# Kernel tuning notes

Hardware: AMD Instinct MI355X
Metric: run time of the kernel (lower is better)

The kernel has to match this reference:

```python
import jax, jax.numpy as jnp
import numpy as np

BS, L, D, N, K = 2048, 100, 256, 16, 32
M_CONST = 2
NEG = -1e9


def setup_inputs() -> dict:
    key = jax.random.key(0)
    ks = jax.random.split(key, 6)
    hist = jax.random.normal(ks[0], (BS, L, D), dtype=jnp.float32)
    hist_mask = jnp.ones((BS, L), dtype=jnp.float32)  # passed but unused by PolyAttention (faithful)
    cand = jax.random.normal(ks[1], (BS, N, D), dtype=jnp.float32)
    num_interests = jax.random.randint(ks[2], (BS,), 1, K + 1, dtype=jnp.int32)
    cat_counts = jax.random.randint(ks[3], (BS,), 1, 21, dtype=jnp.int32)
    W_poly = jax.random.normal(ks[4], (D, D), dtype=jnp.float32) * (1.0 / np.sqrt(D))
    context_codes = jax.random.normal(ks[5], (K, D), dtype=jnp.float32) * (1.0 / np.sqrt(D))
    return {
        "history_news_representations": hist,
        "history_mask": hist_mask,
        "candidate_news_representations": cand,
        "num_extracted_interests": num_interests,
        "unique_category_counts": cat_counts,
        "W_poly": W_poly,
        "context_codes": context_codes,
    }


def _forward(hist, hist_mask, cand, num_interests, cat_counts, W_poly, context_codes):
    # --- PolyAttention ---
    proj = jnp.tanh(jnp.einsum("bld,ed->ble", hist, W_poly))        # [bs, L, ccd]
    weights = jnp.einsum("ble,ke->bkl", proj, context_codes)         # [bs, K, L]
    cc_mask = jnp.arange(K)[None, :] < num_interests[:, None]        # [bs, K]
    weights = jnp.where(cc_mask[:, :, None], weights, NEG)
    weights = jax.nn.softmax(weights, axis=2)
    weights = jnp.nan_to_num(weights, nan=0.0, posinf=0.0, neginf=0.0)
    interests = jnp.einsum("bkl,bld->bkd", weights, hist)            # [bs, K, d]

    # --- InterestCandidateAttention over all N candidates at once ---
    aw = jnp.einsum("bkd,bnd->bnk", interests, cand)                 # [bs, N, K]
    dyn_K = jnp.ceil(jnp.log2(M_CONST * cat_counts.astype(jnp.float32))).astype(jnp.int32)
    dyn_K = jnp.clip(dyn_K, 1, K)                                    # [bs]
    # rank of each entry in descending order along K
    order = jnp.argsort(-aw, axis=-1)
    rank = jnp.argsort(order, axis=-1)                               # [bs, N, K]
    topk_mask = (rank < dyn_K[:, None, None]).astype(aw.dtype)
    masked = aw * topk_mask
    user = jnp.einsum("bnk,bkd->bnd", masked, interests)             # [bs, N, d]
    return user


def reference(history_news_representations, history_mask, candidate_news_representations,
              num_extracted_interests, unique_category_counts, W_poly, context_codes):
    return _forward(history_news_representations, history_mask, candidate_news_representations,
                    num_extracted_interests, unique_category_counts, W_poly, context_codes)
```

## Files before the change

kernel.cpp:

```cpp
#include <hip/hip_runtime.h>
#include <math.h>

#define NEGV (-1e9f)

typedef _Float16 half8 __attribute__((ext_vector_type(8)));
typedef float f32x4 __attribute__((ext_vector_type(4)));


__device__ inline float tanh_fast(float x) {
    float t = __expf(2.0f * x);
    float r = __builtin_amdgcn_rcpf(t + 1.0f);
    return fmaf(-2.0f, r, 1.0f);
}

__device__ inline void split8(const float4 a, const float4 b, half8& h, half8& m) {
    const float* pa = (const float*)&a;
    const float* pb = (const float*)&b;
    #pragma unroll
    for (int q = 0; q < 4; ++q) {
        float x = pa[q];
        _Float16 hi = (_Float16)x;
        h[q] = hi; m[q] = (_Float16)(x - (float)hi);
    }
    #pragma unroll
    for (int q = 0; q < 4; ++q) {
        float x = pb[q];
        _Float16 hi = (_Float16)x;
        h[4+q] = hi; m[4+q] = (_Float16)(x - (float)hi);
    }
}

__device__ inline void gload_lds16(const void* g, void* lds) {
    __builtin_amdgcn_global_load_lds(
        (const __attribute__((address_space(1))) unsigned int*)g,
        (__attribute__((address_space(3))) unsigned int*)lds, 16, 0, 0);
}

__global__ __launch_bounds__(256)
void k_prep(const float* __restrict__ W, const float* __restrict__ cc,
            half8* __restrict__ Wf, half8* __restrict__ Cf)
{
    int slot = blockIdx.x * 256 + threadIdx.x;
    if (slot < 8192) {
        int kt = slot >> 10;
        int ct = (slot >> 6) & 15;
        int lane = slot & 63;
        int e = ct * 16 + (lane & 15);
        int g = lane >> 4;
        const float* src = &W[(size_t)e * 256 + kt * 32 + g * 8];
        float4 a = *(const float4*)src;
        float4 b = *(const float4*)(src + 4);
        half8 h, m;
        split8(a, b, h, m);
        Wf[((kt * 2 + 0) * 16 + ct) * 64 + lane] = h;
        Wf[((kt * 2 + 1) * 16 + ct) * 64 + lane] = m;
    } else if (slot < 9216) {
        int s = slot - 8192;
        int lane = s & 63;
        int ct = (s >> 6) & 1;
        int et = s >> 7;
        int k2 = ct * 16 + (lane & 15);
        int g = lane >> 4;
        const float* src = &cc[(size_t)k2 * 256 + et * 32 + g * 8];
        float4 a = *(const float4*)src;
        float4 b = *(const float4*)(src + 4);
        half8 h, m;
        split8(a, b, h, m);
        Cf[((et * 2 + 0) * 2 + ct) * 64 + lane] = h;
        Cf[((et * 2 + 1) * 2 + ct) * 64 + lane] = m;
    }
}

__global__ __launch_bounds__(512, 2)
void k_proj_logits(const float* __restrict__ hist, const half8* __restrict__ Wf,
                   const half8* __restrict__ Cf, float* __restrict__ logits)
{
    __shared__ __align__(16) char smem[65536];
    float (*Pj)[68] = (float(*)[68])smem;

    const int tid  = threadIdx.x;
    const int lane = tid & 63;
    const int w    = tid >> 6;
    const int wr   = w >> 1, wc = w & 1;
    const int g    = lane >> 4;
    const int r    = lane & 15;
    const size_t rowBase = (size_t)blockIdx.x * 256;

    f32x4 acc[4][8];
    #pragma unroll
    for (int i = 0; i < 4; ++i)
        #pragma unroll
        for (int j = 0; j < 8; ++j) acc[i][j] = (f32x4)(0.0f);

    const float* aPtr = &hist[(rowBase + (size_t)wr * 64 + r) * 256 + g * 8];
    const char*  wsrc = (const char*)Wf + tid * 16;
    const int    ldsW = (tid & 448) * 16;

    float4 a0[4], a1[4];
    #pragma unroll
    for (int rt = 0; rt < 4; ++rt) {
        const float* s = aPtr + rt * (16 * 256);
        a0[rt] = *(const float4*)s;
        a1[rt] = *(const float4*)(s + 4);
    }
    #pragma unroll
    for (int i = 0; i < 4; ++i)
        gload_lds16(wsrc + i * 8192, smem + ldsW + i * 8192);
    __syncthreads();

    #pragma unroll 2
    for (int kt = 0; kt < 8; ++kt) {
        const int cur = kt & 1;
        if (kt < 7) {
            const char* s = wsrc + (size_t)(kt + 1) * 32768;
            char* d = smem + (cur ^ 1) * 32768 + ldsW;
            #pragma unroll
            for (int i = 0; i < 4; ++i)
                gload_lds16(s + i * 8192, d + i * 8192);
        }
        half8 Ah[4], Am[4];
        #pragma unroll
        for (int rt = 0; rt < 4; ++rt)
            split8(a0[rt], a1[rt], Ah[rt], Am[rt]);
        if (kt < 7) {
            #pragma unroll
            for (int rt = 0; rt < 4; ++rt) {
                const float* s = aPtr + rt * (16 * 256) + (kt + 1) * 32;
                a0[rt] = *(const float4*)s;
                a1[rt] = *(const float4*)(s + 4);
            }
        }
        __builtin_amdgcn_sched_barrier(0);

        const _Float16* Bf = (const _Float16*)(smem + cur * 32768);
        #pragma unroll
        for (int ct = 0; ct < 8; ++ct) {
            int ctg = wc * 8 + ct;
            half8 Bh = *(const half8*)&Bf[(( 0 + ctg) * 64 + lane) * 8];
            half8 Bm = *(const half8*)&Bf[((16 + ctg) * 64 + lane) * 8];
            #pragma unroll
            for (int rt = 0; rt < 4; ++rt) {
                acc[rt][ct] = __builtin_amdgcn_mfma_f32_16x16x32_f16(Ah[rt], Bh, acc[rt][ct], 0, 0, 0);
                acc[rt][ct] = __builtin_amdgcn_mfma_f32_16x16x32_f16(Ah[rt], Bm, acc[rt][ct], 0, 0, 0);
                acc[rt][ct] = __builtin_amdgcn_mfma_f32_16x16x32_f16(Am[rt], Bh, acc[rt][ct], 0, 0, 0);
            }
        }
        __syncthreads();
    }

    #pragma unroll
    for (int p = 0; p < 2; ++p) {
        f32x4 acc2[2];
        acc2[0] = (f32x4)(0.0f);
        acc2[1] = (f32x4)(0.0f);
        #pragma unroll
        for (int ec = 0; ec < 4; ++ec) {
            __syncthreads();
            if ((wr >> 1) == p && wc == (ec >> 1)) {
                #pragma unroll
                for (int rt = 0; rt < 4; ++rt) {
                    #pragma unroll
                    for (int c4i = 0; c4i < 4; ++c4i) {
                        int ctm = (ec & 1) * 4 + c4i;
                        f32x4 t = acc[rt][ctm];
                        int el = c4i * 16 + r;
                        int rb = (wr & 1) * 64 + rt * 16 + g * 4;
                        #pragma unroll
                        for (int i = 0; i < 4; ++i)
                            Pj[rb + i][el] = tanh_fast(t[i]);
                    }
                }
            }
            __syncthreads();
            #pragma unroll
            for (int ks = 0; ks < 2; ++ks) {
                half8 Ah2, Am2;
                {
                    const float* src = &Pj[w * 16 + r][ks * 32 + g * 8];
                    float4 p0 = *(const float4*)src;
                    float4 p1 = *(const float4*)(src + 4);
                    split8(p0, p1, Ah2, Am2);
                }
                int et = ec * 2 + ks;
                #pragma unroll
                for (int ct = 0; ct < 2; ++ct) {
                    half8 Bh = Cf[((et * 2 + 0) * 2 + ct) * 64 + lane];
                    half8 Bm = Cf[((et * 2 + 1) * 2 + ct) * 64 + lane];
                    acc2[ct] = __builtin_amdgcn_mfma_f32_16x16x32_f16(Ah2, Bh, acc2[ct], 0, 0, 0);
                    acc2[ct] = __builtin_amdgcn_mfma_f32_16x16x32_f16(Ah2, Bm, acc2[ct], 0, 0, 0);
                    acc2[ct] = __builtin_amdgcn_mfma_f32_16x16x32_f16(Am2, Bh, acc2[ct], 0, 0, 0);
                }
            }
        }
        #pragma unroll
        for (int ct = 0; ct < 2; ++ct)
            #pragma unroll
            for (int i = 0; i < 4; ++i) {
                size_t grow = rowBase + p * 128 + w * 16 + g * 4 + i;
                logits[grow * 32 + ct * 16 + r] = acc2[ct][i];
            }
    }
}

__global__ __launch_bounds__(256, 3)
void k_attn(const float* __restrict__ hist, const float* __restrict__ cand,
            const int* __restrict__ numi, const int* __restrict__ catc,
            const float* __restrict__ logits, float* __restrict__ out)
{
    __shared__ float wT[100][36];
    __shared__ float ints[32][260];
    __shared__ float aws[16][36];
    __shared__ float maw[16][36];

    const int tid = threadIdx.x;
    const int b = blockIdx.x;
    const int num = numi[b];

    for (int idx = tid; idx < 3200; idx += 256) {
        int l = idx >> 5;
        int k = idx & 31;
        wT[l][k] = logits[(size_t)b * 3200 + idx];
    }
    __syncthreads();

    {
        const int k = tid >> 3;
        const int lg = tid & 7;
        const bool valid = k < num;
        float vals[13];
        float m = -INFINITY;
        #pragma unroll
        for (int i = 0; i < 13; ++i) {
            int l = lg + 8 * i;
            if (l < 100) {
                float v = valid ? wT[l][k] : NEGV;
                vals[i] = v;
                m = fmaxf(m, v);
            }
        }
        #pragma unroll
        for (int off = 1; off < 8; off <<= 1)
            m = fmaxf(m, __shfl_xor(m, off, 8));
        float s = 0.0f;
        #pragma unroll
        for (int i = 0; i < 13; ++i) {
            int l = lg + 8 * i;
            if (l < 100) {
                float e = expf(vals[i] - m);
                s += e;
                wT[l][k] = e;
            }
        }
        #pragma unroll
        for (int off = 1; off < 8; off <<= 1)
            s += __shfl_xor(s, off, 8);
        float inv = 1.0f / s;
        #pragma unroll
        for (int i = 0; i < 13; ++i) {
            int l = lg + 8 * i;
            if (l < 100) wT[l][k] *= inv;
        }
    }
    __syncthreads();

    {
        const int dq = tid & 63;
        const int kh = tid >> 6;
        float4 a4[8];
        #pragma unroll
        for (int kk = 0; kk < 8; ++kk) { a4[kk].x = a4[kk].y = a4[kk].z = a4[kk].w = 0.0f; }
        const float4* hrow = (const float4*)&hist[(size_t)b * 25600] + dq;
        #pragma unroll 4
        for (int l = 0; l < 100; ++l) {
            float4 hv = hrow[(size_t)l * 64];
            float4 w0 = *(const float4*)&wT[l][8 * kh];
            float4 w1 = *(const float4*)&wT[l][8 * kh + 4];
            float wv[8] = {w0.x, w0.y, w0.z, w0.w, w1.x, w1.y, w1.z, w1.w};
            #pragma unroll
            for (int kk = 0; kk < 8; ++kk) {
                a4[kk].x = fmaf(wv[kk], hv.x, a4[kk].x);
                a4[kk].y = fmaf(wv[kk], hv.y, a4[kk].y);
                a4[kk].z = fmaf(wv[kk], hv.z, a4[kk].z);
                a4[kk].w = fmaf(wv[kk], hv.w, a4[kk].w);
            }
        }
        #pragma unroll
        for (int kk = 0; kk < 8; ++kk)
            *(float4*)&ints[8 * kh + kk][4 * dq] = a4[kk];
    }
    __syncthreads();

    {
        const int n = tid & 15;
        const int kq = tid >> 4;
        const float4* cg = (const float4*)&cand[((size_t)b * 16 + n) * 256];
        const float4* i0 = (const float4*)&ints[kq][0];
        const float4* i1 = (const float4*)&ints[kq + 16][0];
        float s0 = 0.0f, s1 = 0.0f;
        for (int q = 0; q < 64; ++q) {
            float4 cv = cg[q];
            float4 v0 = i0[q];
            float4 v1 = i1[q];
            s0 += v0.x * cv.x + v0.y * cv.y + v0.z * cv.z + v0.w * cv.w;
            s1 += v1.x * cv.x + v1.y * cv.y + v1.z * cv.z + v1.w * cv.w;
        }
        aws[n][kq] = s0;
        aws[n][kq + 16] = s1;
    }
    __syncthreads();

    {
        int c = catc[b];
        int dynK = 32 - __clz(2 * c - 1);
        const int k = tid & 31;
        const int n1 = tid >> 5;
        #pragma unroll
        for (int h = 0; h < 2; ++h) {
            int n = n1 + 8 * h;
            float a = aws[n][k];
            int cnt = 0;
            #pragma unroll
            for (int j = 0; j < 32; ++j) {
                float aj = aws[n][j];
                cnt += (aj > a) || (aj == a && j < k);
            }
            maw[n][k] = (cnt < dynK) ? a : 0.0f;
        }
    }
    __syncthreads();

    {
        const int dd = tid & 63;
        const int ng = tid >> 6;
        float4 acc4[4];
        #pragma unroll
        for (int nn = 0; nn < 4; ++nn) { acc4[nn].x = acc4[nn].y = acc4[nn].z = acc4[nn].w = 0.0f; }
        for (int k = 0; k < 32; ++k) {
            float4 iv = *(const float4*)&ints[k][4 * dd];
            #pragma unroll
            for (int nn = 0; nn < 4; ++nn) {
                float m = maw[4 * ng + nn][k];
                acc4[nn].x = fmaf(m, iv.x, acc4[nn].x);
                acc4[nn].y = fmaf(m, iv.y, acc4[nn].y);
                acc4[nn].z = fmaf(m, iv.z, acc4[nn].z);
                acc4[nn].w = fmaf(m, iv.w, acc4[nn].w);
            }
        }
        #pragma unroll
        for (int nn = 0; nn < 4; ++nn) {
            *(float4*)&out[((size_t)b * 16 + 4 * ng + nn) * 256 + 4 * dd] = acc4[nn];
        }
    }
}

extern "C" void kernel_launch(void* const* d_in, const int* in_sizes, int n_in,
                              void* d_out, int out_size, void* d_ws, size_t ws_size,
                              hipStream_t stream) {
    const float* hist = (const float*)d_in[0];
    const float* cand = (const float*)d_in[2];
    const int*   numi = (const int*)d_in[3];
    const int*   catc = (const int*)d_in[4];
    const float* W    = (const float*)d_in[5];
    const float* cc   = (const float*)d_in[6];
    float* out = (float*)d_out;
    float* logits = (float*)d_ws;
    const size_t LOG_BYTES = 26214400;
    const size_t WF_BYTES = 262144;
    const size_t CF_BYTES = 32768;
    char* fragBase = (ws_size >= LOG_BYTES + WF_BYTES + CF_BYTES)
                     ? ((char*)d_ws + LOG_BYTES)
                     : (char*)d_out;
    half8* Wf = (half8*)fragBase;
    half8* Cf = (half8*)(fragBase + WF_BYTES);

    k_prep<<<36, 256, 0, stream>>>(W, cc, Wf, Cf);
    k_proj_logits<<<800, 512, 0, stream>>>(hist, Wf, Cf, logits);
    k_attn<<<2048, 256, 0, stream>>>(hist, cand, numi, catc, logits, out);
}
```

Baseline: 276.7 us.

## Interleave projection GEMM with fine-grained barriers, packed fp16 split, and aliased attention LDS

The projection GEMM main loop is split into four sub-phases per k-tile. Each sub-phase loads B fragments ahead, raises wave priority around the MFMA bursts, and uses explicit vmcnt waits and raw s_barriers instead of full __syncthreads. The fp32-to-fp16 hi/lo split now uses packed cvt_pkrtz conversions, which switch rounding to round-toward-zero and may shift accuracy slightly. The attention kernel aliases the wT and ints shared buffers, adding one barrier, so its LDS footprint drops enough to allow 4 blocks per CU instead of 3.

```diff
diff --git a/kernel.cpp b/kernel.cpp
--- a/kernel.cpp
+++ b/kernel.cpp
@@ -4,6 +4,7 @@
 #define NEGV (-1e9f)
 
 typedef _Float16 half8 __attribute__((ext_vector_type(8)));
+typedef __fp16 fp16x2 __attribute__((ext_vector_type(2)));
 typedef float f32x4 __attribute__((ext_vector_type(4)));
 
 
@@ -14,19 +15,15 @@
 }
 
 __device__ inline void split8(const float4 a, const float4 b, half8& h, half8& m) {
-    const float* pa = (const float*)&a;
-    const float* pb = (const float*)&b;
+    const float x[8] = {a.x, a.y, a.z, a.w, b.x, b.y, b.z, b.w};
     #pragma unroll
     for (int q = 0; q < 4; ++q) {
-        float x = pa[q];
-        _Float16 hi = (_Float16)x;
-        h[q] = hi; m[q] = (_Float16)(x - (float)hi);
-    }
-    #pragma unroll
-    for (int q = 0; q < 4; ++q) {
-        float x = pb[q];
-        _Float16 hi = (_Float16)x;
-        h[4+q] = hi; m[4+q] = (_Float16)(x - (float)hi);
+        fp16x2 hp = __builtin_amdgcn_cvt_pkrtz(x[2 * q], x[2 * q + 1]);
+        float r0 = x[2 * q]     - (float)hp[0];
+        float r1 = x[2 * q + 1] - (float)hp[1];
+        fp16x2 mp = __builtin_amdgcn_cvt_pkrtz(r0, r1);
+        h[2 * q] = (_Float16)hp[0]; h[2 * q + 1] = (_Float16)hp[1];
+        m[2 * q] = (_Float16)mp[0]; m[2 * q + 1] = (_Float16)mp[1];
     }
 }
 
@@ -106,46 +103,65 @@
     #pragma unroll
     for (int i = 0; i < 4; ++i)
         gload_lds16(wsrc + i * 8192, smem + ldsW + i * 8192);
-    __syncthreads();
-
-    #pragma unroll 2
+    __builtin_amdgcn_sched_barrier(0);
+    asm volatile("s_waitcnt vmcnt(0)" ::: "memory");
+    __builtin_amdgcn_s_barrier();
+    __builtin_amdgcn_sched_barrier(0);
+
     for (int kt = 0; kt < 8; ++kt) {
         const int cur = kt & 1;
-        if (kt < 7) {
-            const char* s = wsrc + (size_t)(kt + 1) * 32768;
-            char* d = smem + (cur ^ 1) * 32768 + ldsW;
-            #pragma unroll
-            for (int i = 0; i < 4; ++i)
-                gload_lds16(s + i * 8192, d + i * 8192);
-        }
+        const _Float16* Bf = (const _Float16*)(smem + cur * 32768);
         half8 Ah[4], Am[4];
         #pragma unroll
-        for (int rt = 0; rt < 4; ++rt)
-            split8(a0[rt], a1[rt], Ah[rt], Am[rt]);
-        if (kt < 7) {
-            #pragma unroll
-            for (int rt = 0; rt < 4; ++rt) {
-                const float* s = aPtr + rt * (16 * 256) + (kt + 1) * 32;
-                a0[rt] = *(const float4*)s;
-                a1[rt] = *(const float4*)(s + 4);
-            }
-        }
-        __builtin_amdgcn_sched_barrier(0);
-
-        const _Float16* Bf = (const _Float16*)(smem + cur * 32768);
-        #pragma unroll
-        for (int ct = 0; ct < 8; ++ct) {
-            int ctg = wc * 8 + ct;
-            half8 Bh = *(const half8*)&Bf[(( 0 + ctg) * 64 + lane) * 8];
-            half8 Bm = *(const half8*)&Bf[((16 + ctg) * 64 + lane) * 8];
-            #pragma unroll
-            for (int rt = 0; rt < 4; ++rt) {
-                acc[rt][ct] = __builtin_amdgcn_mfma_f32_16x16x32_f16(Ah[rt], Bh, acc[rt][ct], 0, 0, 0);
-                acc[rt][ct] = __builtin_amdgcn_mfma_f32_16x16x32_f16(Ah[rt], Bm, acc[rt][ct], 0, 0, 0);
-                acc[rt][ct] = __builtin_amdgcn_mfma_f32_16x16x32_f16(Am[rt], Bh, acc[rt][ct], 0, 0, 0);
-            }
-        }
-        __syncthreads();
+        for (int p = 0; p < 4; ++p) {
+            half8 Bh[2], Bm[2];
+            #pragma unroll
+            for (int c = 0; c < 2; ++c) {
+                int ctg = wc * 8 + 2 * p + c;
+                Bh[c] = *(const half8*)&Bf[(( 0 + ctg) * 64 + lane) * 8];
+                Bm[c] = *(const half8*)&Bf[((16 + ctg) * 64 + lane) * 8];
+            }
+            if (p == 0) {
+                if (kt < 7) {
+                    const char* s = wsrc + (size_t)(kt + 1) * 32768;
+                    char* d = smem + (cur ^ 1) * 32768 + ldsW;
+                    #pragma unroll
+                    for (int i = 0; i < 4; ++i)
+                        gload_lds16(s + i * 8192, d + i * 8192);
+                }
+                #pragma unroll
+                for (int rt = 0; rt < 4; ++rt)
+                    split8(a0[rt], a1[rt], Ah[rt], Am[rt]);
+                if (kt < 7) {
+                    #pragma unroll
+                    for (int rt = 0; rt < 4; ++rt) {
+                        const float* s = aPtr + rt * (16 * 256) + (kt + 1) * 32;
+                        a0[rt] = *(const float4*)s;
+                        a1[rt] = *(const float4*)(s + 4);
+                    }
+                }
+            }
+            if (p == 3) {
+                __builtin_amdgcn_sched_barrier(0);
+                if (kt < 7) asm volatile("s_waitcnt vmcnt(8)" ::: "memory");
+                else        asm volatile("s_waitcnt vmcnt(0)" ::: "memory");
+            }
+            __builtin_amdgcn_s_barrier();
+            __builtin_amdgcn_sched_barrier(0);
+            __builtin_amdgcn_s_setprio(1);
+            #pragma unroll
+            for (int c = 0; c < 2; ++c) {
+                int ct = 2 * p + c;
+                #pragma unroll
+                for (int rt = 0; rt < 4; ++rt) {
+                    acc[rt][ct] = __builtin_amdgcn_mfma_f32_16x16x32_f16(Ah[rt], Bh[c], acc[rt][ct], 0, 0, 0);
+                    acc[rt][ct] = __builtin_amdgcn_mfma_f32_16x16x32_f16(Ah[rt], Bm[c], acc[rt][ct], 0, 0, 0);
+                    acc[rt][ct] = __builtin_amdgcn_mfma_f32_16x16x32_f16(Am[rt], Bh[c], acc[rt][ct], 0, 0, 0);
+                }
+            }
+            __builtin_amdgcn_s_setprio(0);
+            __builtin_amdgcn_s_barrier();
+        }
     }
 
     #pragma unroll
@@ -202,15 +218,16 @@
     }
 }
 
-__global__ __launch_bounds__(256, 3)
+__global__ __launch_bounds__(256, 4)
 void k_attn(const float* __restrict__ hist, const float* __restrict__ cand,
             const int* __restrict__ numi, const int* __restrict__ catc,
             const float* __restrict__ logits, float* __restrict__ out)
 {
-    __shared__ float wT[100][36];
-    __shared__ float ints[32][260];
-    __shared__ float aws[16][36];
-    __shared__ float maw[16][36];
+    __shared__ __align__(16) char smem[37888];
+    float (*ints)[260] = (float(*)[260])smem;
+    float (*wT)[36]    = (float(*)[36])smem;
+    float (*aws)[36]   = (float(*)[36])(smem + 33280);
+    float (*maw)[36]   = (float(*)[36])(smem + 35584);
 
     const int tid = threadIdx.x;
     const int b = blockIdx.x;
@@ -284,6 +301,7 @@
                 a4[kk].w = fmaf(wv[kk], hv.w, a4[kk].w);
             }
         }
+        __syncthreads();
         #pragma unroll
         for (int kk = 0; kk < 8; ++kk)
             *(float4*)&ints[8 * kh + kk][4 * dq] = a4[kk];
```

After: 279.1 us. Within noise of the previous version (+0.9%).
